# Kernel tuning notes

Hardware: AMD Instinct MI355X
Metric: run time of the kernel (lower is better)

The kernel has to match this reference:

```python
import jax, jax.numpy as jnp
import numpy as np

DIM = 64
N_NODES = 20000
N_EDGES = 60000
N_TORS = 1024
ACT = 6


def setup_inputs() -> dict:
    key = jax.random.key(0)
    ks = iter(jax.random.split(key, 40))
    def rn(*s):
        return jax.random.normal(next(ks), s, dtype=jnp.float32) * 0.05
    d = DIM
    inp = {}
    inp["x"] = jax.random.normal(next(ks), (N_NODES, 3), dtype=jnp.float32)
    inp["edge_attr"] = jax.random.uniform(next(ks), (N_EDGES, 7), dtype=jnp.float32)
    inp["W0"] = rn(d, 3); inp["b0"] = rn(d)
    inp["We1"] = rn(128, 7); inp["be1"] = rn(128)
    inp["We2"] = rn(d * d, 128); inp["be2"] = rn(d * d)
    inp["root"] = rn(d, d); inp["conv_b"] = rn(d)
    inp["gru_wih"] = rn(3 * d, d); inp["gru_whh"] = rn(3 * d, d)
    inp["gru_bih"] = rn(3 * d); inp["gru_bhh"] = rn(3 * d)
    inp["s2s_wi"] = rn(4 * d, 2 * d); inp["s2s_wh"] = rn(4 * d, d)
    inp["s2s_bi"] = rn(4 * d); inp["s2s_bh"] = rn(4 * d)
    inp["mem_wi"] = rn(24 * d, 6 * d); inp["mem_wh"] = rn(24 * d, 6 * d)
    inp["mem_bi"] = rn(24 * d); inp["mem_bh"] = rn(24 * d)
    inp["W1"] = rn(2 * d, 6 * d); inp["b1"] = rn(2 * d)
    inp["W2"] = rn(ACT, 2 * d); inp["b2"] = rn(ACT)
    inp["edge_index"] = jax.random.randint(next(ks), (2, N_EDGES), 0, N_NODES)
    inp["nonring"] = jax.random.randint(next(ks), (N_TORS, 4), 0, N_NODES)
    return inp


def reference(x, edge_attr, W0, b0, We1, be1, We2, be2, root, conv_b,
              gru_wih, gru_whh, gru_bih, gru_bhh,
              s2s_wi, s2s_wh, s2s_bi, s2s_bh,
              mem_wi, mem_wh, mem_bi, mem_bh,
              W1, b1, W2, b2, edge_index, nonring):
    d = DIM
    n = x.shape[0]
    src, dst = edge_index[0], edge_index[1]
    # lin0 + relu
    out = jax.nn.relu(x @ W0.T + b0)                       # [N, d]
    h = out                                                # GRU hidden
    # per-edge dim x dim weights from the edge MLP (edge_attr is loop-invariant)
    We = jax.nn.relu(edge_attr @ We1.T + be1) @ We2.T + be2
    We = We.reshape(-1, d, d)                              # [E, d, d]
    deg = jnp.zeros((n,), jnp.float32).at[dst].add(1.0)
    inv_deg = 1.0 / jnp.maximum(deg, 1.0)
    for _ in range(6):
        # NNConv: gather -> per-edge matmul -> scatter-mean, plus root transform
        msg = jnp.einsum('ed,edf->ef', out[src], We)       # [E, d]
        agg = jnp.zeros((n, d), msg.dtype).at[dst].add(msg) * inv_deg[:, None]
        m = jax.nn.relu(agg + out @ root + conv_b)
        # GRU cell (torch gate order r, z, n)
        gx = m @ gru_wih.T + gru_bih
        gh = h @ gru_whh.T + gru_bhh
        r = jax.nn.sigmoid(gx[:, :d] + gh[:, :d])
        z = jax.nn.sigmoid(gx[:, d:2 * d] + gh[:, d:2 * d])
        nn_ = jnp.tanh(gx[:, 2 * d:] + r * gh[:, 2 * d:])
        h = (1.0 - z) * nn_ + z * h
        out = h
    # Set2Set pooling, single graph (data.batch is all zeros)
    q_star = jnp.zeros((1, 2 * d), out.dtype)
    hs = jnp.zeros((1, d), out.dtype)
    cs = jnp.zeros((1, d), out.dtype)
    for _ in range(6):
        g = q_star @ s2s_wi.T + s2s_bi + hs @ s2s_wh.T + s2s_bh
        i = jax.nn.sigmoid(g[:, :d])
        f = jax.nn.sigmoid(g[:, d:2 * d])
        gg = jnp.tanh(g[:, 2 * d:3 * d])
        o = jax.nn.sigmoid(g[:, 3 * d:])
        cs = f * cs + i * gg
        hs = o * jnp.tanh(cs)
        q = hs                                             # [1, d]
        e = out @ q[0]                                     # [N]
        a = jax.nn.softmax(e)
        rvec = (a[:, None] * out).sum(0, keepdims=True)    # [1, d]
        q_star = jnp.concatenate([q, rvec], axis=1)
    pool = q_star                                          # [1, 2d]
    # faithful quirky index/view/permute + repeat_interleave concat
    t = nonring.shape[0]
    sel = out[nonring.reshape(-1)]                         # [4T, d]
    sel = sel.reshape(4 * d, t).T                          # [T, 4d]
    rep = jnp.repeat(pool.reshape(-1), t).reshape(t, 2 * d)
    z_in = jnp.concatenate([sel, rep], axis=1)             # [T, 6d]
    # memory LSTM, seq_len = 1, zero initial state (states not passed in orig)
    D6 = 6 * d
    g = z_in @ mem_wi.T + mem_bi + mem_bh                  # h0 = 0 so Wh term vanishes
    i = jax.nn.sigmoid(g[:, :D6])
    f = jax.nn.sigmoid(g[:, D6:2 * D6])
    gg = jnp.tanh(g[:, 2 * D6:3 * D6])
    o = jax.nn.sigmoid(g[:, 3 * D6:])
    cm = i * gg
    hm = o * jnp.tanh(cm)                                  # [T, 6d]
    y = jax.nn.relu(hm @ W1.T + b1) @ W2.T + b2            # [T, ACT]
    return y[None]                                         # [1, T, ACT]
```

## Files before the change

kernel.cpp:

```cpp
#include <hip/hip_runtime.h>
#include <hip/hip_bf16.h>

#define NN 20000
#define NE 60000
#define NT 1024

typedef unsigned short ushortT;
typedef __attribute__((ext_vector_type(8))) short bf16x8;
typedef __attribute__((ext_vector_type(8))) unsigned short u16x8;
typedef __attribute__((ext_vector_type(4))) float f32x4;

__device__ __forceinline__ float sigm(float x){ return 1.0f/(1.0f+expf(-x)); }
__device__ __forceinline__ float bfu2f(ushortT u){ return __uint_as_float(((unsigned)u)<<16); }
__device__ __forceinline__ ushortT f2bfu(float f){
  __hip_bfloat16 b = __float2bfloat16(f);
  return *reinterpret_cast<ushortT*>(&b);
}

__global__ void k_lin0(const float* __restrict__ x, const float* __restrict__ W0,
                       const float* __restrict__ b0, float* __restrict__ out,
                       float* __restrict__ h, ushortT* __restrict__ outbf,
                       ushortT* __restrict__ hbf){
  int idx = blockIdx.x*256 + threadIdx.x;
  int n = idx >> 6, j = idx & 63;
  float a = b0[j] + x[n*3+0]*W0[j*3+0] + x[n*3+1]*W0[j*3+1] + x[n*3+2]*W0[j*3+2];
  a = fmaxf(a, 0.0f);
  out[idx] = a; h[idx] = a;
  ushortT u = f2bfu(a);
  outbf[idx] = u; hbf[idx] = u;
}

__global__ void k_deg(const int* __restrict__ dst, float* __restrict__ deg){
  int e = blockIdx.x*256 + threadIdx.x;
  if (e < NE) atomicAdd(&deg[dst[e]], 1.0f);
}

__global__ void k_edgemlp(const float* __restrict__ ea, const float* __restrict__ We1,
                          const float* __restrict__ be1, ushortT* __restrict__ Rbf){
  int idx = blockIdx.x*256 + threadIdx.x;
  int e = idx >> 7, k = idx & 127;
  float a = be1[k];
  #pragma unroll
  for (int j = 0; j < 7; ++j) a += ea[e*7+j]*We1[k*7+j];
  Rbf[idx] = f2bfu(fmaxf(a, 0.0f));
}

#define PREP_T ((4096*128) + (1536*384) + (128*384) + (192*64) + (192*64) + (64*64))
__global__ void k_prep(const float* __restrict__ We2, const float* __restrict__ memwi,
                       const float* __restrict__ W1, const float* __restrict__ gwih,
                       const float* __restrict__ gwhh, const float* __restrict__ root,
                       ushortT* __restrict__ We2bf, ushortT* __restrict__ wmem,
                       ushortT* __restrict__ w1bf, ushortT* __restrict__ gwihbf,
                       ushortT* __restrict__ gwhhbf, ushortT* __restrict__ rootTbf){
  int idx = blockIdx.x*256 + threadIdx.x;
  if (idx < 4096*128){ We2bf[idx] = f2bfu(We2[idx]); return; }
  idx -= 4096*128;
  if (idx < 1536*384){ wmem[idx] = f2bfu(memwi[idx]); return; }
  idx -= 1536*384;
  if (idx < 128*384){ w1bf[idx] = f2bfu(W1[idx]); return; }
  idx -= 128*384;
  if (idx < 192*64){ gwihbf[idx] = f2bfu(gwih[idx]); return; }
  idx -= 192*64;
  if (idx < 192*64){ gwhhbf[idx] = f2bfu(gwhh[idx]); return; }
  idx -= 192*64;
  if (idx < 64*64){ int d = idx >> 6, j = idx & 63; rootTbf[j*64 + d] = f2bfu(root[idx]); }
}

#define EB 256
__global__ __launch_bounds__(256, 2) void k_fmsg(
    const ushortT* __restrict__ Rbf, const ushortT* __restrict__ We2bf,
    const float* __restrict__ be2, const ushortT* __restrict__ outbf,
    const int* __restrict__ src, const int* __restrict__ dst,
    float* __restrict__ agg)
{
  __shared__ ushortT o_sT[64][264];
  __shared__ ushortT bufB[4][4096];
  __shared__ float   be2q[64][32];
  __shared__ int     dst_s[EB];

  int tid = threadIdx.x;
  int e0 = blockIdx.x * EB;
  int fh = blockIdx.y;
  int w = tid >> 6, lane = tid & 63;
  int l15 = lane & 15, g = lane >> 4;

  auto stage = [&](int d, int b){
    #pragma unroll
    for (int i = 0; i < 2; ++i){
      int s = (w*2 + i)*64 + lane;
      int row = s >> 4, kslot = s & 15;
      const ushortT* gp = We2bf + (size_t)((d<<6) + (fh<<5) + row)*128 + ((kslot ^ (row & 7))<<3);
      __builtin_amdgcn_global_load_lds(
          (const __attribute__((address_space(1))) void*)gp,
          (__attribute__((address_space(3))) void*)&bufB[b][(size_t)s*8], 16, 0, 0);
    }
  };
  stage(0, 0); stage(1, 1);

  {
    int ge = e0 + tid;
    int sn = src[ge];
    dst_s[tid] = (ge < NE) ? dst[ge] : -1;
    const ushortT* op = outbf + (size_t)sn*64;
    #pragma unroll
    for (int i = 0; i < 8; ++i){
      u16x8 v = *reinterpret_cast<const u16x8*>(op + i*8);
      #pragma unroll
      for (int j = 0; j < 8; ++j) o_sT[i*8+j][tid] = v[j];
    }
  }
  #pragma unroll
  for (int i = 0; i < 8; ++i){
    int idx = tid*8 + i;
    int dd = idx >> 5, cc = idx & 31;
    be2q[dd][cc] = be2[(dd<<6) + (fh<<5) + cc];
  }

  bf16x8 af[4][4];
  #pragma unroll
  for (int t = 0; t < 4; ++t){
    #pragma unroll
    for (int ks = 0; ks < 4; ++ks){
      int ge = e0 + w*64 + t*16 + l15;
      bf16x8 z = {0,0,0,0,0,0,0,0};
      af[t][ks] = (ge < NE) ? *reinterpret_cast<const bf16x8*>(Rbf + (size_t)ge*128 + ks*32 + g*8) : z;
    }
  }

  f32x4 msg[4][2];
  #pragma unroll
  for (int t = 0; t < 4; ++t){
    #pragma unroll
    for (int q = 0; q < 2; ++q){ msg[t][q][0]=0.f; msg[t][q][1]=0.f; msg[t][q][2]=0.f; msg[t][q][3]=0.f; }
  }
  __syncthreads();

  auto compute = [&](int d, int b){
    bf16x8 bf0[4], bf1[4];
    #pragma unroll
    for (int ks = 0; ks < 4; ++ks){
      bf0[ks] = *reinterpret_cast<const bf16x8*>(&bufB[b][ (l15)*128    + ((((ks<<2)+g) ^ (l15&7))<<3) ]);
      bf1[ks] = *reinterpret_cast<const bf16x8*>(&bufB[b][ (16+l15)*128 + ((((ks<<2)+g) ^ (l15&7))<<3) ]);
    }
    f32x4 ac[4][2];
    #pragma unroll
    for (int t = 0; t < 4; ++t){
      #pragma unroll
      for (int q = 0; q < 2; ++q){ ac[t][q][0]=0.f; ac[t][q][1]=0.f; ac[t][q][2]=0.f; ac[t][q][3]=0.f; }
    }
    __builtin_amdgcn_s_setprio(1);
    #pragma unroll
    for (int ks = 0; ks < 4; ++ks){
      #pragma unroll
      for (int t = 0; t < 4; ++t){
        ac[t][0] = __builtin_amdgcn_mfma_f32_16x16x32_bf16(af[t][ks], bf0[ks], ac[t][0], 0, 0, 0);
        ac[t][1] = __builtin_amdgcn_mfma_f32_16x16x32_bf16(af[t][ks], bf1[ks], ac[t][1], 0, 0, 0);
      }
    }
    __builtin_amdgcn_s_setprio(0);
    float be2v0 = be2q[d][l15];
    float be2v1 = be2q[d][16 + l15];
    #pragma unroll
    for (int t = 0; t < 4; ++t){
      ushort4 ou = *reinterpret_cast<const ushort4*>(&o_sT[d][w*64 + t*16 + g*4]);
      float o0 = bfu2f(ou.x), o1 = bfu2f(ou.y), o2 = bfu2f(ou.z), o3 = bfu2f(ou.w);
      msg[t][0][0] += o0*(ac[t][0][0] + be2v0);
      msg[t][0][1] += o1*(ac[t][0][1] + be2v0);
      msg[t][0][2] += o2*(ac[t][0][2] + be2v0);
      msg[t][0][3] += o3*(ac[t][0][3] + be2v0);
      msg[t][1][0] += o0*(ac[t][1][0] + be2v1);
      msg[t][1][1] += o1*(ac[t][1][1] + be2v1);
      msg[t][1][2] += o2*(ac[t][1][2] + be2v1);
      msg[t][1][3] += o3*(ac[t][1][3] + be2v1);
    }
  };

  for (int p = 0; p < 32; ++p){
    int d0 = p << 1;
    asm volatile("s_waitcnt vmcnt(0)" ::: "memory");
    __builtin_amdgcn_sched_barrier(0);
    __builtin_amdgcn_s_barrier();
    __builtin_amdgcn_sched_barrier(0);
    if (p < 31){
      stage(d0 + 2, (d0 + 2) & 3);
      stage(d0 + 3, (d0 + 3) & 3);
    }
    compute(d0,     d0 & 3);
    compute(d0 + 1, (d0 + 1) & 3);
  }

  #pragma unroll
  for (int t = 0; t < 4; ++t){
    #pragma unroll
    for (int r = 0; r < 4; ++r){
      int el = w*64 + t*16 + g*4 + r;
      int tn = dst_s[el];
      if (tn >= 0){
        atomicAdd(&agg[(size_t)tn*64 + (fh<<5) + l15],      msg[t][0][r]);
        atomicAdd(&agg[(size_t)tn*64 + (fh<<5) + 16 + l15], msg[t][1][r]);
      }
    }
  }
}

__global__ __launch_bounds__(256) void k_gru2(
    const float* __restrict__ agg_in, const float* __restrict__ deg,
    const ushortT* __restrict__ rootT, const float* __restrict__ conv_b,
    const ushortT* __restrict__ wih, const ushortT* __restrict__ whh,
    const float* __restrict__ bih, const float* __restrict__ bhh,
    float* __restrict__ out, float* __restrict__ h,
    ushortT* __restrict__ outbf, ushortT* __restrict__ hbf)
{
  __shared__ ushortT mbf[32*64];
  float* agg = const_cast<float*>(agg_in);
  int tid = threadIdx.x;
  int w = tid >> 6, lane = tid & 63;
  int l15 = lane & 15, g = lane >> 4;
  int n0 = blockIdx.x * 32;
  int j = w*16 + l15;

  f32x4 acc1[2];
  #pragma unroll
  for (int rt = 0; rt < 2; ++rt){ acc1[rt][0]=0.f; acc1[rt][1]=0.f; acc1[rt][2]=0.f; acc1[rt][3]=0.f; }
  bf16x8 ah[2][2];
  #pragma unroll
  for (int ks = 0; ks < 2; ++ks){
    bf16x8 b = *reinterpret_cast<const bf16x8*>(rootT + (size_t)j*64 + g*8 + ks*32);
    #pragma unroll
    for (int rt = 0; rt < 2; ++rt){
      bf16x8 a = *reinterpret_cast<const bf16x8*>(outbf + (size_t)(n0 + rt*16 + l15)*64 + g*8 + ks*32);
      acc1[rt] = __builtin_amdgcn_mfma_f32_16x16x32_bf16(a, b, acc1[rt], 0, 0, 0);
      ah[rt][ks] = *reinterpret_cast<const bf16x8*>(hbf + (size_t)(n0 + rt*16 + l15)*64 + g*8 + ks*32);
    }
  }
  {
    float cb = conv_b[j];
    #pragma unroll
    for (int rt = 0; rt < 2; ++rt){
      #pragma unroll
      for (int r = 0; r < 4; ++r){
        int row = rt*16 + g*4 + r;
        int node = n0 + row;
        float inv = 1.0f/fmaxf(deg[node], 1.0f);
        float mval = fmaxf(acc1[rt][r] + agg[(size_t)node*64 + j]*inv + cb, 0.0f);
        agg[(size_t)node*64 + j] = 0.0f;
        int gran = (j >> 3) ^ (row & 7);
        mbf[row*64 + (gran<<3) + (j & 7)] = f2bfu(mval);
      }
    }
  }
  __syncthreads();

  f32x4 gx[3][2], gh[3][2];
  #pragma unroll
  for (int ci = 0; ci < 3; ++ci){
    #pragma unroll
    for (int rt = 0; rt < 2; ++rt){
      gx[ci][rt][0]=0.f; gx[ci][rt][1]=0.f; gx[ci][rt][2]=0.f; gx[ci][rt][3]=0.f;
      gh[ci][rt][0]=0.f; gh[ci][rt][1]=0.f; gh[ci][rt][2]=0.f; gh[ci][rt][3]=0.f;
    }
  }
  #pragma unroll
  for (int ks = 0; ks < 2; ++ks){
    bf16x8 am[2];
    #pragma unroll
    for (int rt = 0; rt < 2; ++rt){
      int arow = rt*16 + l15;
      int agran = (g + ks*4) ^ (l15 & 7);
      am[rt] = *reinterpret_cast<const bf16x8*>(&mbf[arow*64 + (agran<<3)]);
    }
    #pragma unroll
    for (int ci = 0; ci < 3; ++ci){
      int c = (w + ci*4)*16 + l15;
      bf16x8 bx = *reinterpret_cast<const bf16x8*>(wih + (size_t)c*64 + g*8 + ks*32);
      bf16x8 bh = *reinterpret_cast<const bf16x8*>(whh + (size_t)c*64 + g*8 + ks*32);
      #pragma unroll
      for (int rt = 0; rt < 2; ++rt){
        gx[ci][rt] = __builtin_amdgcn_mfma_f32_16x16x32_bf16(am[rt], bx, gx[ci][rt], 0, 0, 0);
        gh[ci][rt] = __builtin_amdgcn_mfma_f32_16x16x32_bf16(ah[rt][ks], bh, gh[ci][rt], 0, 0, 0);
      }
    }
  }
  float bxr = bih[j], bxz = bih[64+j], bxn = bih[128+j];
  float bhr = bhh[j], bhz = bhh[64+j], bhn = bhh[128+j];
  #pragma unroll
  for (int rt = 0; rt < 2; ++rt){
    #pragma unroll
    for (int r = 0; r < 4; ++r){
      int node = n0 + rt*16 + g*4 + r;
      float gxr = gx[0][rt][r] + bxr, gxz = gx[1][rt][r] + bxz, gxn = gx[2][rt][r] + bxn;
      float ghr = gh[0][rt][r] + bhr, ghz = gh[1][rt][r] + bhz, ghn = gh[2][rt][r] + bhn;
      float rr = sigm(gxr + ghr), zz = sigm(gxz + ghz);
      float nn_ = tanhf(gxn + rr*ghn);
      float hold = h[(size_t)node*64 + j];
      float hn = (1.0f - zz)*nn_ + zz*hold;
      h[(size_t)node*64 + j]   = hn;
      out[(size_t)node*64 + j] = hn;
      ushortT u = f2bfu(hn);
      outbf[(size_t)node*64 + j] = u;
      hbf[(size_t)node*64 + j]   = u;
    }
  }
}

__global__ void k_s2s2(const float* __restrict__ out, const float* __restrict__ wi,
                       const float* __restrict__ wh, const float* __restrict__ bi,
                       const float* __restrict__ bh, float* __restrict__ st, int it){
  const float* sr = st + it*256;
  float* sw = st + (it+1)*256;
  __shared__ float qs[128], hsl[64], gg[256];
  __shared__ float ob[128*65], wl[128], zred[128], part[256];
  int tid = threadIdx.x;
  int n0 = blockIdx.x * 128;

  if (tid < 64) qs[tid] = sr[tid];
  else if (tid < 128){
    float Z = sr[192];
    qs[tid] = (Z != 0.0f) ? sr[128 + (tid-64)]/Z : 0.0f;
  }
  __syncthreads();
  {
    float a = bi[tid] + bh[tid];
    #pragma unroll 8
    for (int k = 0; k < 128; ++k) a += qs[k]*wi[tid*128 + k];
    #pragma unroll 8
    for (int k = 0; k < 64;  ++k) a += sr[k]*wh[tid*64 + k];
    gg[tid] = a;
  }
  __syncthreads();
  if (tid < 64){
    float iv = sigm(gg[tid]), fv = sigm(gg[64+tid]);
    float gv = tanhf(gg[128+tid]), ov = sigm(gg[192+tid]);
    float c = fv*sr[64+tid] + iv*gv;
    float hnew = ov*tanhf(c);
    hsl[tid] = hnew;
    if (blockIdx.x == 0){ sw[64+tid] = c; sw[tid] = hnew; }
  }
  #pragma unroll
  for (int rr = 0; rr < 8; ++rr){
    int idx = rr*1024 + tid*4;
    int nl = idx >> 6, jj = idx & 63;
    float4 v = make_float4(0.f,0.f,0.f,0.f);
    if (n0 + nl < NN) v = *reinterpret_cast<const float4*>(&out[(size_t)(n0+nl)*64 + jj]);
    ob[nl*65 + jj + 0] = v.x; ob[nl*65 + jj + 1] = v.y;
    ob[nl*65 + jj + 2] = v.z; ob[nl*65 + jj + 3] = v.w;
  }
  __syncthreads();
  if (tid < 128){
    float e = 0.f;
    #pragma unroll 8
    for (int jj = 0; jj < 64; ++jj) e += ob[tid*65 + jj]*hsl[jj];
    float wv = (n0 + tid < NN) ? expf(e) : 0.f;
    wl[tid] = wv; zred[tid] = wv;
  }
  __syncthreads();
  if (tid < 64) zred[tid] += zred[tid + 64];
  __syncthreads();
  if (tid < 32) zred[tid] += zred[tid + 32];
  __syncthreads();
  if (tid < 16) zred[tid] += zred[tid + 16];
  __syncthreads();
  if (tid < 8) zred[tid] += zred[tid + 8];
  __syncthreads();
  if (tid == 0){
    float z = zred[0]+zred[1]+zred[2]+zred[3]+zred[4]+zred[5]+zred[6]+zred[7];
    atomicAdd(&sw[192], z);
  }
  {
    int gq = tid >> 6, d = tid & 63;
    float acc = 0.f;
    #pragma unroll 8
    for (int i = 0; i < 32; ++i){
      int nl = gq*32 + i;
      acc += wl[nl]*ob[nl*65 + d];
    }
    part[tid] = acc;
  }
  __syncthreads();
  if (tid < 64)
    atomicAdd(&sw[128 + tid], part[tid] + part[64+tid] + part[128+tid] + part[192+tid]);
}

__global__ void k_z(const float* __restrict__ out, const float* __restrict__ st,
                    const int* __restrict__ nonring, ushortT* __restrict__ zbf){
  const float* s6 = st + 6*256;
  int idx = blockIdx.x*256 + threadIdx.x;
  int t = idx / 384, c = idx % 384;
  float v;
  if (c < 256){
    int a = c*16 + (t >> 6);
    int node = nonring[a];
    v = out[(size_t)node*64 + (t & 63)];
  } else {
    int pi = t >> 3;
    v = (pi < 64) ? s6[pi] : s6[128 + (pi - 64)] / s6[192];
  }
  zbf[idx] = f2bfu(v);
}

__global__ __launch_bounds__(256) void k_mem2(
    const ushortT* __restrict__ zbf, const ushortT* __restrict__ wmem,
    const float* __restrict__ membi, const float* __restrict__ membh,
    ushortT* __restrict__ hmbf){
  int tid = threadIdx.x;
  int w = tid >> 6, lane = tid & 63;
  int l15 = lane & 15, g = lane >> 4;
  int m0 = blockIdx.x * 32;
  int jw = blockIdx.y * 64 + w * 16;

  f32x4 ai[2], ag[2], ao[2];
  #pragma unroll
  for (int m = 0; m < 2; ++m){
    #pragma unroll
    for (int r = 0; r < 4; ++r){ ai[m][r]=0.f; ag[m][r]=0.f; ao[m][r]=0.f; }
  }
  const ushortT* a0p = zbf + (size_t)(m0 + l15)*384 + g*8;
  const ushortT* a1p = zbf + (size_t)(m0 + 16 + l15)*384 + g*8;
  const ushortT* bip = wmem + (size_t)(jw + l15)*384 + g*8;
  const ushortT* bgp = wmem + (size_t)(768 + jw + l15)*384 + g*8;
  const ushortT* bop = wmem + (size_t)(1152 + jw + l15)*384 + g*8;
  #pragma unroll
  for (int ks = 0; ks < 12; ++ks){
    bf16x8 a0 = *reinterpret_cast<const bf16x8*>(a0p + ks*32);
    bf16x8 a1 = *reinterpret_cast<const bf16x8*>(a1p + ks*32);
    bf16x8 bi = *reinterpret_cast<const bf16x8*>(bip + ks*32);
    bf16x8 bg = *reinterpret_cast<const bf16x8*>(bgp + ks*32);
    bf16x8 bo = *reinterpret_cast<const bf16x8*>(bop + ks*32);
    ai[0] = __builtin_amdgcn_mfma_f32_16x16x32_bf16(a0, bi, ai[0], 0, 0, 0);
    ai[1] = __builtin_amdgcn_mfma_f32_16x16x32_bf16(a1, bi, ai[1], 0, 0, 0);
    ag[0] = __builtin_amdgcn_mfma_f32_16x16x32_bf16(a0, bg, ag[0], 0, 0, 0);
    ag[1] = __builtin_amdgcn_mfma_f32_16x16x32_bf16(a1, bg, ag[1], 0, 0, 0);
    ao[0] = __builtin_amdgcn_mfma_f32_16x16x32_bf16(a0, bo, ao[0], 0, 0, 0);
    ao[1] = __builtin_amdgcn_mfma_f32_16x16x32_bf16(a1, bo, ao[1], 0, 0, 0);
  }
  int j = jw + l15;
  float bI = membi[j]        + membh[j];
  float bG = membi[768 + j]  + membh[768 + j];
  float bO = membi[1152 + j] + membh[1152 + j];
  #pragma unroll
  for (int m = 0; m < 2; ++m){
    #pragma unroll
    for (int r = 0; r < 4; ++r){
      int t = m0 + m*16 + g*4 + r;
      float gi = ai[m][r] + bI;
      float gG = ag[m][r] + bG;
      float go = ao[m][r] + bO;
      float cm = sigm(gi)*tanhf(gG);
      hmbf[(size_t)t*384 + j] = f2bfu(sigm(go)*tanhf(cm));
    }
  }
}

__global__ __launch_bounds__(256) void k_fin1(
    const ushortT* __restrict__ hmbf, const ushortT* __restrict__ w1bf,
    const float* __restrict__ b1, float* __restrict__ hid){
  int tid = threadIdx.x;
  int w = tid >> 6, lane = tid & 63;
  int l15 = lane & 15, g = lane >> 4;
  int m0 = blockIdx.x * 32;
  int cw = blockIdx.y * 64 + w * 16;

  f32x4 acc[2];
  #pragma unroll
  for (int m = 0; m < 2; ++m){
    #pragma unroll
    for (int r = 0; r < 4; ++r) acc[m][r] = 0.f;
  }
  const ushortT* a0p = hmbf + (size_t)(m0 + l15)*384 + g*8;
  const ushortT* a1p = hmbf + (size_t)(m0 + 16 + l15)*384 + g*8;
  const ushortT* bp  = w1bf + (size_t)(cw + l15)*384 + g*8;
  #pragma unroll
  for (int ks = 0; ks < 12; ++ks){
    bf16x8 a0 = *reinterpret_cast<const bf16x8*>(a0p + ks*32);
    bf16x8 a1 = *reinterpret_cast<const bf16x8*>(a1p + ks*32);
    bf16x8 b  = *reinterpret_cast<const bf16x8*>(bp + ks*32);
    acc[0] = __builtin_amdgcn_mfma_f32_16x16x32_bf16(a0, b, acc[0], 0, 0, 0);
    acc[1] = __builtin_amdgcn_mfma_f32_16x16x32_bf16(a1, b, acc[1], 0, 0, 0);
  }
  int c = cw + l15;
  float bv = b1[c];
  #pragma unroll
  for (int m = 0; m < 2; ++m){
    #pragma unroll
    for (int r = 0; r < 4; ++r){
      int t = m0 + m*16 + g*4 + r;
      hid[(size_t)t*128 + c] = fmaxf(acc[m][r] + bv, 0.0f);
    }
  }
}

__global__ void k_fin2(const float* __restrict__ hid, const float* __restrict__ W2,
                       const float* __restrict__ b2, float* __restrict__ y){
  int tid = threadIdx.x;
  int t = blockIdx.x*32 + (tid >> 3);
  int j = tid & 7;
  if (j >= 6) return;
  float a = b2[j];
  const float* hp = hid + (size_t)t*128;
  const float* wp = W2 + j*128;
  #pragma unroll 8
  for (int k = 0; k < 128; ++k) a += hp[k]*wp[k];
  y[t*6 + j] = a;
}

extern "C" void kernel_launch(void* const* d_in, const int* in_sizes, int n_in,
                              void* d_out, int out_size, void* d_ws, size_t ws_size,
                              hipStream_t stream){
  const float* x      = (const float*)d_in[0];
  const float* ea     = (const float*)d_in[1];
  const float* W0     = (const float*)d_in[2];
  const float* b0     = (const float*)d_in[3];
  const float* We1    = (const float*)d_in[4];
  const float* be1    = (const float*)d_in[5];
  const float* We2    = (const float*)d_in[6];
  const float* be2    = (const float*)d_in[7];
  const float* root   = (const float*)d_in[8];
  const float* conv_b = (const float*)d_in[9];
  const float* gwih   = (const float*)d_in[10];
  const float* gwhh   = (const float*)d_in[11];
  const float* gbih   = (const float*)d_in[12];
  const float* gbhh   = (const float*)d_in[13];
  const float* s2swi  = (const float*)d_in[14];
  const float* s2swh  = (const float*)d_in[15];
  const float* s2sbi  = (const float*)d_in[16];
  const float* s2sbh  = (const float*)d_in[17];
  const float* memwi  = (const float*)d_in[18];
  const float* membi  = (const float*)d_in[20];
  const float* membh  = (const float*)d_in[21];
  const float* W1     = (const float*)d_in[22];
  const float* b1     = (const float*)d_in[23];
  const float* W2     = (const float*)d_in[24];
  const float* b2     = (const float*)d_in[25];
  const int*   eidx   = (const int*)d_in[26];
  const int*   nonr   = (const int*)d_in[27];
  const int* src = eidx, *dst = eidx + NE;
  float* y = (float*)d_out;

  char* wsb = (char*)d_ws;
  size_t off = 0;
  auto alloc = [&](size_t bytes){ size_t o = off; off += (bytes + 255) & ~(size_t)255; return o; };
  float* out    = (float*)(wsb + alloc((size_t)NN*64*4));
  float* h      = (float*)(wsb + alloc((size_t)NN*64*4));
  float* agg    = (float*)(wsb + alloc((size_t)NN*64*4));
  float* deg    = (float*)(wsb + alloc((size_t)NN*4));
  float* st     = (float*)(wsb + alloc(7*256*4));
  float* hid    = (float*)(wsb + alloc((size_t)NT*128*4));
  ushortT* Rbf  = (ushortT*)(wsb + alloc((size_t)NE*128*2));
  ushortT* We2bf= (ushortT*)(wsb + alloc((size_t)4096*128*2));
  ushortT* wmem = (ushortT*)(wsb + alloc((size_t)1536*384*2));
  ushortT* w1bf = (ushortT*)(wsb + alloc((size_t)128*384*2));
  ushortT* zbf  = (ushortT*)(wsb + alloc((size_t)NT*384*2));
  ushortT* hmbf = (ushortT*)(wsb + alloc((size_t)NT*384*2));
  ushortT* outbf= (ushortT*)(wsb + alloc((size_t)NN*64*2));
  ushortT* hbf  = (ushortT*)(wsb + alloc((size_t)NN*64*2));
  ushortT* gwihbf = (ushortT*)(wsb + alloc((size_t)192*64*2));
  ushortT* gwhhbf = (ushortT*)(wsb + alloc((size_t)192*64*2));
  ushortT* rootTbf= (ushortT*)(wsb + alloc((size_t)64*64*2));
  (void)ws_size; (void)n_in; (void)in_sizes; (void)out_size;

  hipMemsetAsync(deg, 0, (size_t)NN*4, stream);
  hipMemsetAsync(st, 0, 7*256*4, stream);
  hipMemsetAsync(agg, 0, (size_t)NN*64*4, stream);
  k_lin0<<<NN*64/256, 256, 0, stream>>>(x, W0, b0, out, h, outbf, hbf);
  k_deg<<<(NE+255)/256, 256, 0, stream>>>(dst, deg);
  k_edgemlp<<<NE*128/256, 256, 0, stream>>>(ea, We1, be1, Rbf);
  k_prep<<<(PREP_T+255)/256, 256, 0, stream>>>(We2, memwi, W1, gwih, gwhh, root,
                                               We2bf, wmem, w1bf, gwihbf, gwhhbf, rootTbf);

  for (int it = 0; it < 6; ++it){
    k_fmsg<<<dim3((NE + EB - 1)/EB, 2), 256, 0, stream>>>(Rbf, We2bf, be2, outbf, src, dst, agg);
    k_gru2<<<NN/32, 256, 0, stream>>>(agg, deg, rootTbf, conv_b, gwihbf, gwhhbf,
                                      gbih, gbhh, out, h, outbf, hbf);
  }

  for (int it = 0; it < 6; ++it){
    k_s2s2<<<(NN + 127)/128, 256, 0, stream>>>(out, s2swi, s2swh, s2sbi, s2sbh, st, it);
  }

  k_z<<<NT*384/256, 256, 0, stream>>>(out, st, nonr, zbf);
  k_mem2<<<dim3(32, 6), 256, 0, stream>>>(zbf, wmem, membi, membh, hmbf);
  k_fin1<<<dim3(32, 2), 256, 0, stream>>>(hmbf, w1bf, b1, hid);
  k_fin2<<<32, 256, 0, stream>>>(hid, W2, b2, y);
}
```

Measured before the change: 674.4 us.

## Restructure edge-message kernel: per-wave output-feature slices with private double buffers, no block barriers

The edge-message kernel now processes 128 edges per block, and each wave owns a 16-wide slice of the 64 output features. Previously the block covered 256 edges and the grid was split into two feature halves. Each wave streams its own We2 slice into a private double buffer and waits on a partial vmcnt, so the per-step block-wide barrier is gone. The A fragments are reused across eight edge tiles, which removes the duplicated gather and A loads of the old two-way feature split. The cost is more A-fragment registers per thread and a shallower prefetch depth.

```diff
diff --git a/kernel.cpp b/kernel.cpp
--- a/kernel.cpp
+++ b/kernel.cpp
@@ -66,139 +66,116 @@
   if (idx < 64*64){ int d = idx >> 6, j = idx & 63; rootTbf[j*64 + d] = f2bfu(root[idx]); }
 }
 
-#define EB 256
+#define EB 128
 __global__ __launch_bounds__(256, 2) void k_fmsg(
     const ushortT* __restrict__ Rbf, const ushortT* __restrict__ We2bf,
     const float* __restrict__ be2, const ushortT* __restrict__ outbf,
     const int* __restrict__ src, const int* __restrict__ dst,
     float* __restrict__ agg)
 {
-  __shared__ ushortT o_sT[64][264];
-  __shared__ ushortT bufB[4][4096];
-  __shared__ float   be2q[64][32];
+  __shared__ ushortT o_sT[64][136];
+  __shared__ ushortT bufB[4][2][2048];
+  __shared__ float   be2q[64][64];
   __shared__ int     dst_s[EB];
 
   int tid = threadIdx.x;
   int e0 = blockIdx.x * EB;
-  int fh = blockIdx.y;
   int w = tid >> 6, lane = tid & 63;
   int l15 = lane & 15, g = lane >> 4;
+  int f = (w << 4) + l15;
 
   auto stage = [&](int d, int b){
     #pragma unroll
-    for (int i = 0; i < 2; ++i){
-      int s = (w*2 + i)*64 + lane;
+    for (int i = 0; i < 4; ++i){
+      int s = i*64 + lane;
       int row = s >> 4, kslot = s & 15;
-      const ushortT* gp = We2bf + (size_t)((d<<6) + (fh<<5) + row)*128 + ((kslot ^ (row & 7))<<3);
+      const ushortT* gp = We2bf + (size_t)((d<<6) + (w<<4) + row)*128 + ((kslot ^ (row & 7))<<3);
       __builtin_amdgcn_global_load_lds(
           (const __attribute__((address_space(1))) void*)gp,
-          (__attribute__((address_space(3))) void*)&bufB[b][(size_t)s*8], 16, 0, 0);
+          (__attribute__((address_space(3))) void*)&bufB[w][b][(size_t)i*512], 16, 0, 0);
     }
   };
-  stage(0, 0); stage(1, 1);
+  stage(0, 0);
 
   {
-    int ge = e0 + tid;
-    int sn = src[ge];
-    dst_s[tid] = (ge < NE) ? dst[ge] : -1;
-    const ushortT* op = outbf + (size_t)sn*64;
-    #pragma unroll
-    for (int i = 0; i < 8; ++i){
+    int ei = tid >> 1;
+    int ge = e0 + ei;
+    int sn = (ge < NE) ? src[ge] : 0;
+    if (tid < EB) dst_s[tid] = (e0 + tid < NE) ? dst[e0 + tid] : -1;
+    int half = (tid & 1) * 32;
+    const ushortT* op = outbf + (size_t)sn*64 + half;
+    #pragma unroll
+    for (int i = 0; i < 4; ++i){
       u16x8 v = *reinterpret_cast<const u16x8*>(op + i*8);
       #pragma unroll
-      for (int j = 0; j < 8; ++j) o_sT[i*8+j][tid] = v[j];
-    }
-  }
-  #pragma unroll
-  for (int i = 0; i < 8; ++i){
-    int idx = tid*8 + i;
-    int dd = idx >> 5, cc = idx & 31;
-    be2q[dd][cc] = be2[(dd<<6) + (fh<<5) + cc];
-  }
-
-  bf16x8 af[4][4];
-  #pragma unroll
-  for (int t = 0; t < 4; ++t){
+      for (int j = 0; j < 8; ++j) o_sT[half + i*8 + j][ei] = v[j];
+    }
+  }
+  #pragma unroll
+  for (int i = 0; i < 4; ++i){
+    int idx = tid*16 + i*4;
+    *reinterpret_cast<float4*>(&be2q[0][0] + idx) =
+        *reinterpret_cast<const float4*>(be2 + idx);
+  }
+
+  bf16x8 af[8][4];
+  #pragma unroll
+  for (int t = 0; t < 8; ++t){
     #pragma unroll
     for (int ks = 0; ks < 4; ++ks){
-      int ge = e0 + w*64 + t*16 + l15;
+      int ge = e0 + t*16 + l15;
       bf16x8 z = {0,0,0,0,0,0,0,0};
       af[t][ks] = (ge < NE) ? *reinterpret_cast<const bf16x8*>(Rbf + (size_t)ge*128 + ks*32 + g*8) : z;
     }
   }
 
-  f32x4 msg[4][2];
-  #pragma unroll
-  for (int t = 0; t < 4; ++t){
-    #pragma unroll
-    for (int q = 0; q < 2; ++q){ msg[t][q][0]=0.f; msg[t][q][1]=0.f; msg[t][q][2]=0.f; msg[t][q][3]=0.f; }
-  }
-  __syncthreads();
-
-  auto compute = [&](int d, int b){
-    bf16x8 bf0[4], bf1[4];
-    #pragma unroll
-    for (int ks = 0; ks < 4; ++ks){
-      bf0[ks] = *reinterpret_cast<const bf16x8*>(&bufB[b][ (l15)*128    + ((((ks<<2)+g) ^ (l15&7))<<3) ]);
-      bf1[ks] = *reinterpret_cast<const bf16x8*>(&bufB[b][ (16+l15)*128 + ((((ks<<2)+g) ^ (l15&7))<<3) ]);
-    }
-    f32x4 ac[4][2];
-    #pragma unroll
-    for (int t = 0; t < 4; ++t){
-      #pragma unroll
-      for (int q = 0; q < 2; ++q){ ac[t][q][0]=0.f; ac[t][q][1]=0.f; ac[t][q][2]=0.f; ac[t][q][3]=0.f; }
-    }
+  f32x4 msg[8];
+  #pragma unroll
+  for (int t = 0; t < 8; ++t){ msg[t][0]=0.f; msg[t][1]=0.f; msg[t][2]=0.f; msg[t][3]=0.f; }
+  __syncthreads();
+
+  for (int d = 0; d < 64; ++d){
+    if (d < 63) stage(d + 1, (d + 1) & 1);
+    if (d < 63){
+      asm volatile("s_waitcnt vmcnt(4)" ::: "memory");
+    } else {
+      asm volatile("s_waitcnt vmcnt(0)" ::: "memory");
+    }
+    __builtin_amdgcn_sched_barrier(0);
+    int b = d & 1;
+    bf16x8 bf[4];
+    #pragma unroll
+    for (int ks = 0; ks < 4; ++ks)
+      bf[ks] = *reinterpret_cast<const bf16x8*>(&bufB[w][b][ l15*128 + ((((ks<<2)+g) ^ (l15&7))<<3) ]);
+    f32x4 ac[8];
+    #pragma unroll
+    for (int t = 0; t < 8; ++t){ ac[t][0]=0.f; ac[t][1]=0.f; ac[t][2]=0.f; ac[t][3]=0.f; }
     __builtin_amdgcn_s_setprio(1);
     #pragma unroll
     for (int ks = 0; ks < 4; ++ks){
       #pragma unroll
-      for (int t = 0; t < 4; ++t){
-        ac[t][0] = __builtin_amdgcn_mfma_f32_16x16x32_bf16(af[t][ks], bf0[ks], ac[t][0], 0, 0, 0);
-        ac[t][1] = __builtin_amdgcn_mfma_f32_16x16x32_bf16(af[t][ks], bf1[ks], ac[t][1], 0, 0, 0);
-      }
+      for (int t = 0; t < 8; ++t)
+        ac[t] = __builtin_amdgcn_mfma_f32_16x16x32_bf16(af[t][ks], bf[ks], ac[t], 0, 0, 0);
     }
     __builtin_amdgcn_s_setprio(0);
-    float be2v0 = be2q[d][l15];
-    float be2v1 = be2q[d][16 + l15];
-    #pragma unroll
-    for (int t = 0; t < 4; ++t){
-      ushort4 ou = *reinterpret_cast<const ushort4*>(&o_sT[d][w*64 + t*16 + g*4]);
-      float o0 = bfu2f(ou.x), o1 = bfu2f(ou.y), o2 = bfu2f(ou.z), o3 = bfu2f(ou.w);
-      msg[t][0][0] += o0*(ac[t][0][0] + be2v0);
-      msg[t][0][1] += o1*(ac[t][0][1] + be2v0);
-      msg[t][0][2] += o2*(ac[t][0][2] + be2v0);
-      msg[t][0][3] += o3*(ac[t][0][3] + be2v0);
-      msg[t][1][0] += o0*(ac[t][1][0] + be2v1);
-      msg[t][1][1] += o1*(ac[t][1][1] + be2v1);
-      msg[t][1][2] += o2*(ac[t][1][2] + be2v1);
-      msg[t][1][3] += o3*(ac[t][1][3] + be2v1);
-    }
-  };
-
-  for (int p = 0; p < 32; ++p){
-    int d0 = p << 1;
-    asm volatile("s_waitcnt vmcnt(0)" ::: "memory");
-    __builtin_amdgcn_sched_barrier(0);
-    __builtin_amdgcn_s_barrier();
-    __builtin_amdgcn_sched_barrier(0);
-    if (p < 31){
-      stage(d0 + 2, (d0 + 2) & 3);
-      stage(d0 + 3, (d0 + 3) & 3);
-    }
-    compute(d0,     d0 & 3);
-    compute(d0 + 1, (d0 + 1) & 3);
-  }
-
-  #pragma unroll
-  for (int t = 0; t < 4; ++t){
+    float be2v = be2q[d][f];
+    #pragma unroll
+    for (int t = 0; t < 8; ++t){
+      ushort4 ou = *reinterpret_cast<const ushort4*>(&o_sT[d][t*16 + g*4]);
+      msg[t][0] += bfu2f(ou.x)*(ac[t][0] + be2v);
+      msg[t][1] += bfu2f(ou.y)*(ac[t][1] + be2v);
+      msg[t][2] += bfu2f(ou.z)*(ac[t][2] + be2v);
+      msg[t][3] += bfu2f(ou.w)*(ac[t][3] + be2v);
+    }
+  }
+
+  #pragma unroll
+  for (int t = 0; t < 8; ++t){
     #pragma unroll
     for (int r = 0; r < 4; ++r){
-      int el = w*64 + t*16 + g*4 + r;
+      int el = t*16 + g*4 + r;
       int tn = dst_s[el];
-      if (tn >= 0){
-        atomicAdd(&agg[(size_t)tn*64 + (fh<<5) + l15],      msg[t][0][r]);
-        atomicAdd(&agg[(size_t)tn*64 + (fh<<5) + 16 + l15], msg[t][1][r]);
-      }
+      if (tn >= 0) atomicAdd(&agg[(size_t)tn*64 + f], msg[t][r]);
     }
   }
 }
@@ -568,7 +545,7 @@
                                                We2bf, wmem, w1bf, gwihbf, gwhhbf, rootTbf);
 
   for (int it = 0; it < 6; ++it){
-    k_fmsg<<<dim3((NE + EB - 1)/EB, 2), 256, 0, stream>>>(Rbf, We2bf, be2, outbf, src, dst, agg);
+    k_fmsg<<<(NE + EB - 1)/EB, 256, 0, stream>>>(Rbf, We2bf, be2, outbf, src, dst, agg);
     k_gru2<<<NN/32, 256, 0, stream>>>(agg, deg, rootTbf, conv_b, gwihbf, gwhhbf,
                                       gbih, gbhh, out, h, outbf, hbf);
   }
```

Result: no change. 669.8 us (-0.7%).
